# Kernel tuning notes

Measured on AMD Instinct MI355X. Metric: run time of the kernel, lower is better.

## Reference

```python
import jax, jax.numpy as jnp
import numpy as np

MID = 64        # conf.mid_channels
N_INV = 6       # n_layers=8 -> range(1, n_layers-1) -> 6 involution blocks
K = 7           # involution kernel size
GROUP_CH = 16   # RedNet default group_channels
GROUPS = MID // GROUP_CH   # 4
RED = MID // 4             # reduction_ratio = 4 -> 16


def conv2d(x, w, b=None, pad=0):
    out = jax.lax.conv_general_dilated(
        x, w, window_strides=(1, 1), padding=[(pad, pad), (pad, pad)],
        dimension_numbers=('NCHW', 'OIHW', 'NCHW'))
    if b is not None:
        out = out + b[None, :, None, None]
    return out


def extract_patches(x, k):
    # x: (B,C,H,W) -> (B,C,k*k,H,W), same-padded (torch nn.Unfold with pad=k//2)
    p = k // 2
    xp = jnp.pad(x, ((0, 0), (0, 0), (p, p), (p, p)))
    H, W = x.shape[2], x.shape[3]
    slices = [xp[:, :, i:i + H, j:j + W] for i in range(k) for j in range(k)]
    return jnp.stack(slices, axis=2)


def involution(x, red_w, bn_gamma, bn_beta, span_w, span_b):
    # kernel-generation branch: 1x1 conv (no bias) -> BN(eval, mean=0,var=1) -> ReLU -> 1x1 conv
    t = conv2d(x, red_w)                                     # (B,RED,H,W)
    t = bn_gamma[None, :, None, None] * t + bn_beta[None, :, None, None]
    t = jax.nn.relu(t)
    w = conv2d(t, span_w, span_b)                            # (B,K*K*GROUPS,H,W)
    B, _, H, W = w.shape
    w = w.reshape(B, GROUPS, K * K, H, W)
    patches = extract_patches(x, K).reshape(B, GROUPS, GROUP_CH, K * K, H, W)
    out = jnp.einsum('bgkhw,bgckhw->bgchw', w, patches)      # per-pixel dynamic conv
    return out.reshape(B, MID, H, W)


def setup_inputs() -> dict:
    key = jax.random.key(0)
    ks = jax.random.split(key, 12)
    s = 0.05
    inp = {
        'input_tensor': jax.random.normal(ks[0], (1, 3, 128, 128), jnp.float32),
        'conv_in_w': jax.random.normal(ks[1], (MID, 3, 3, 3), jnp.float32) * s,
        'conv_in_b': jax.random.normal(ks[2], (MID,), jnp.float32) * s,
        'red_w': jax.random.normal(ks[3], (N_INV, RED, MID, 1, 1), jnp.float32) * s,
        'bn_gamma': jnp.ones((N_INV, RED), jnp.float32),
        'bn_beta': jnp.zeros((N_INV, RED), jnp.float32),
        'span_w': jax.random.normal(ks[4], (N_INV, K * K * GROUPS, RED, 1, 1), jnp.float32) * s,
        'span_b': jax.random.normal(ks[5], (N_INV, K * K * GROUPS), jnp.float32) * s,
        'conv_out_w': jax.random.normal(ks[6], (12, MID, 3, 3), jnp.float32) * s,
        'conv_out_b': jax.random.normal(ks[7], (12,), jnp.float32) * s,
    }
    return inp


def reference(input_tensor, conv_in_w, conv_in_b, red_w, bn_gamma, bn_beta,
              span_w, span_b, conv_out_w, conv_out_b):
    x = conv2d(input_tensor, conv_in_w, conv_in_b, pad=2)     # (B,MID,H+2,W+2)
    for l in range(N_INV):
        x = jax.nn.relu(involution(x, red_w[l], bn_gamma[l], bn_beta[l],
                                   span_w[l], span_b[l]))
    pixel = conv2d(x, conv_out_w, conv_out_b, pad=0)          # (B,12,H,W)
    # PixelShuffle(2): (B,12,H,W) -> (B,3,2H,2W)
    B, _, H, W = pixel.shape
    out = pixel.reshape(B, 3, 2, 2, H, W).transpose(0, 1, 4, 2, 5, 3)
    return out.reshape(B, 3, 2 * H, 2 * W)
```

## Files before the change

### kernel.cpp

```cpp
#include <hip/hip_runtime.h>


#define HH 130
#define SP 136
#define PPL (SP*SP)
#define GP (PPL*16)
#define XBUF2 (4*GP)
#define TP1 (16900*16)
#define OFF_TA (2*XBUF2)
#define OFF_TB (OFF_TA + 4*TP1)

__global__ __launch_bounds__(256) void conv_in_kernel(
        const float* __restrict__ inf, const float* __restrict__ W,
        const float* __restrict__ b, float* __restrict__ x0,
        float* __restrict__ x1, float* __restrict__ tpA,
        const float* __restrict__ redw0) {
    const int tid = threadIdx.x;
    if (blockIdx.x >= 67) {
        int idx = ((blockIdx.x - 67)*4 + blockIdx.y)*256 + tid;
        if (idx < 3192) {
            int bsel = idx & 1, e = idx >> 1;
            int r, c;
            if (e < 816) { r = e/136; c = e%136; if (r >= 3) r += 130; }
            else { int j = e-816; r = 3 + j/6; int m = j%6; c = (m<3)? m : m+130; }
            float* base = (bsel ? x1 : x0) + ((size_t)r*SP + c)*16;
            float4 z = make_float4(0.f,0.f,0.f,0.f);
            #pragma unroll
            for (int g2 = 0; g2 < 4; ++g2)
                #pragma unroll
                for (int q = 0; q < 4; ++q)
                    *(float4*)(base + (size_t)g2*GP + q*4) = z;
        }
        return;
    }
    __shared__ float wl[448];
    const int g = blockIdx.y;
    for (int i = tid; i < 448; i += 256)
        wl[i] = (i < 432) ? W[g*432 + i] : b[g*16 + (i-432)];
    __syncthreads();
    int px = blockIdx.x*256 + tid;
    int pxc = px < 16900 ? px : 16899;
    int h = pxc/130, w = pxc%130;
    float xv[27];
    #pragma unroll
    for (int i = 0; i < 3; ++i)
      #pragma unroll
      for (int ky = 0; ky < 3; ++ky) {
        int y = h - 2 + ky;
        #pragma unroll
        for (int kx = 0; kx < 3; ++kx) {
            int xx = w - 2 + kx;
            float v = 0.f;
            if ((unsigned)y < 128u && (unsigned)xx < 128u)
                v = inf[i*16384 + y*128 + xx];
            xv[i*9 + ky*3 + kx] = v;
        }
      }
    float acc[16];
    #pragma unroll
    for (int c = 0; c < 16; ++c) {
        float a = wl[432 + c];
        #pragma unroll
        for (int t = 0; t < 27; ++t) a += wl[c*27 + t] * xv[t];
        acc[c] = a;
    }
    if (px < 16900) {
        float* dst = x0 + (size_t)g*GP + ((size_t)(h+3)*SP + (w+3))*16;
        #pragma unroll
        for (int q = 0; q < 4; ++q)
            *(float4*)(dst + q*4) =
                make_float4(acc[q*4], acc[q*4+1], acc[q*4+2], acc[q*4+3]);
        float* td = tpA + (size_t)g*TP1 + (size_t)px*16;
        #pragma unroll
        for (int rq = 0; rq < 4; ++rq) {
            float p0=0.f, p1=0.f, p2=0.f, p3=0.f;
            #pragma unroll
            for (int j = 0; j < 16; ++j) {
                float a = acc[j];
                p0 += redw0[(rq*4+0)*64 + g*16 + j]*a;
                p1 += redw0[(rq*4+1)*64 + g*16 + j]*a;
                p2 += redw0[(rq*4+2)*64 + g*16 + j]*a;
                p3 += redw0[(rq*4+3)*64 + g*16 + j]*a;
            }
            *(float4*)(td + rq*4) = make_float4(p0, p1, p2, p3);
        }
    }
}

#define TL(p, r)  uu[(p)*20 + (r)]
#define WLK(k, p) uu[(k)*68 + (p)]
__global__ __launch_bounds__(256, 5) void e_kernel(
        const float* __restrict__ x,
        const float* __restrict__ tread,
        float* __restrict__ twrite,
        const float* __restrict__ gamma, const float* __restrict__ beta,
        const float* __restrict__ spanw,
        const float* __restrict__ spanb,
        const float* __restrict__ redwn,
        float* __restrict__ xout,
        const int doNext)
{
    __shared__ float xl[4][14][17][4];
    __shared__ float uu[49*68];
    const int wid = blockIdx.x;
    const int slot = wid >> 3;
    const int T = (wid & 7)*37 + (slot >> 2);
    if (T >= 289) return;
    const int g = slot & 3;
    const int ty = (T/17)*8, tx = (T%17)*8;
    const int tid = threadIdx.x;
    const int px = tid & 63;
    const int wv = __builtin_amdgcn_readfirstlane(tid >> 6);
    const int sr = px >> 3, sc = px & 7;

    for (int i = tid; i < 784; i += 256) {
        int q = i & 3, p = i >> 2;
        int r = p / 14, c = p % 14;
        int gr = ty + r, gc = tx + c;
        gr = gr < SP ? gr : SP-1;
        gc = gc < SP ? gc : SP-1;
        float4 v = *(const float4*)(x + (size_t)g*GP
                                    + ((size_t)gr*SP + gc)*16 + q*4);
        *(float4*)&xl[q][r][c][0] = v;
    }

    const int hh = min(ty + sr, HH-1), ww = min(tx + sc, HH-1);
    {
        const size_t toff = ((size_t)hh*HH + ww)*16 + wv*4;
        float4 s = make_float4(0.f,0.f,0.f,0.f);
        #pragma unroll
        for (int gg = 0; gg < 4; ++gg) {
            float4 a = *(const float4*)(tread + (size_t)gg*TP1 + toff);
            s.x += a.x; s.y += a.y; s.z += a.z; s.w += a.w;
        }
        *(float4*)&TL(px, wv*4) = s;
    }
    __syncthreads();

    float t16[16];
    #pragma unroll
    for (int q = 0; q < 4; ++q) {
        float4 v = *(const float4*)&TL(px, q*4);
        t16[q*4+0] = fmaxf(gamma[q*4+0]*v.x + beta[q*4+0], 0.f);
        t16[q*4+1] = fmaxf(gamma[q*4+1]*v.y + beta[q*4+1], 0.f);
        t16[q*4+2] = fmaxf(gamma[q*4+2]*v.z + beta[q*4+2], 0.f);
        t16[q*4+3] = fmaxf(gamma[q*4+3]*v.w + beta[q*4+3], 0.f);
    }
    __syncthreads();

    {
        const float* sw = spanw + g*784;
        const float* sb = spanb + g*49;
        const int k0 = wv ? (wv*12 + 1) : 0;
        #pragma unroll
        for (int j = 0; j < 12; ++j) {
            int k = k0 + j;
            float a = sb[k];
            #pragma unroll
            for (int r = 0; r < 16; ++r) a += sw[k*16 + r] * t16[r];
            WLK(k, px) = a;
        }
        if (wv == 0) {
            float a = sb[12];
            #pragma unroll
            for (int r = 0; r < 16; ++r) a += sw[12*16 + r] * t16[r];
            WLK(12, px) = a;
        }
    }
    __syncthreads();

    const int cq = wv;
    float4 acc = make_float4(0.f, 0.f, 0.f, 0.f);
    #pragma unroll
    for (int i = 0; i < 7; ++i)
        #pragma unroll
        for (int j = 0; j < 7; ++j) {
            float4 xv = *(const float4*)&xl[cq][sr + i][sc + j][0];
            float wk = WLK(i*7 + j, px);
            acc.x += wk*xv.x; acc.y += wk*xv.y;
            acc.z += wk*xv.z; acc.w += wk*xv.w;
        }

    const int h = ty + sr, ww2 = tx + sc;
    const bool valid = (h < HH) && (ww2 < HH);
    float4 o = make_float4(fmaxf(acc.x,0.f), fmaxf(acc.y,0.f),
                           fmaxf(acc.z,0.f), fmaxf(acc.w,0.f));
    if (valid)
        *(float4*)(xout + (size_t)g*GP
                   + ((size_t)(h+3)*SP + (ww2+3))*16 + cq*4) = o;

    if (doNext) {
        float* ol = (float*)xl;
        __syncthreads();
        ol[px*17 + cq*4 + 0] = o.x;
        ol[px*17 + cq*4 + 1] = o.y;
        ol[px*17 + cq*4 + 2] = o.z;
        ol[px*17 + cq*4 + 3] = o.w;
        __syncthreads();
        const int rq = wv;
        float p0=0.f, p1=0.f, p2=0.f, p3=0.f;
        #pragma unroll
        for (int j = 0; j < 16; ++j) {
            float xv = ol[px*17 + j];
            const int c = g*16 + j;
            p0 += redwn[(rq*4+0)*64 + c]*xv;
            p1 += redwn[(rq*4+1)*64 + c]*xv;
            p2 += redwn[(rq*4+2)*64 + c]*xv;
            p3 += redwn[(rq*4+3)*64 + c]*xv;
        }
        if (valid)
            *(float4*)(twrite + (size_t)g*TP1
                       + ((size_t)h*HH + ww2)*16 + rq*4) =
                make_float4(p0, p1, p2, p3);
    }
}

__global__ __launch_bounds__(256) void conv_out_ps_kernel(
        const float* __restrict__ x, const float* __restrict__ W,
        const float* __restrict__ b, float* __restrict__ out)
{
    __shared__ float xh[64*120];
    __shared__ float wl[6912];
    const int tid = threadIdx.x;
    const int ty = blockIdx.y*8, tx = blockIdx.x*8;

    for (int idx = tid; idx < 6912; idx += 256) wl[idx] = W[idx];
    for (int idx = tid; idx < 1600; idx += 256) {
        int g = idx/400, rem = idx%400;
        int p100 = rem>>2, q = rem&3;
        int r = p100/10, cl = p100%10;
        float4 v = *(const float4*)(x + (size_t)g*GP
                     + ((size_t)(ty + r + 3)*SP + tx + cl + 3)*16 + q*4);
        int c0 = g*16 + q*4;
        xh[(c0+0)*120 + r*12 + cl] = v.x;
        xh[(c0+1)*120 + r*12 + cl] = v.y;
        xh[(c0+2)*120 + r*12 + cl] = v.z;
        xh[(c0+3)*120 + r*12 + cl] = v.w;
    }
    __syncthreads();

    const int wave = __builtin_amdgcn_readfirstlane(tid >> 6);
    const int lane = tid & 63;
    const int s = lane >> 2, cq = lane & 3;
    const int sr = s >> 1, pc0 = (s & 1)*4;
    float acc[3][4] = {};

    for (int c = cq*16; c < cq*16 + 16; ++c) {
        #pragma unroll
        for (int ky = 0; ky < 3; ++ky) {
            const float* xb = &xh[c*120 + (sr + ky)*12 + pc0];
            float4 xa = *(const float4*)xb;
            float2 xm = *(const float2*)(xb + 4);
            float xr[6] = {xa.x, xa.y, xa.z, xa.w, xm.x, xm.y};
            #pragma unroll
            for (int oj = 0; oj < 3; ++oj) {
                const float* wp = &wl[((wave*3 + oj)*64 + c)*9 + ky*3];
                #pragma unroll
                for (int kx = 0; kx < 3; ++kx) {
                    float wv = wp[kx];
                    #pragma unroll
                    for (int q = 0; q < 4; ++q)
                        acc[oj][q] += wv * xr[kx + q];
                }
            }
        }
    }

    #pragma unroll
    for (int oj = 0; oj < 3; ++oj)
        #pragma unroll
        for (int q = 0; q < 4; ++q) {
            float v = acc[oj][q];
            v += __shfl_xor(v, 1, 64);
            v += __shfl_xor(v, 2, 64);
            acc[oj][q] = v;
        }

    if (cq == 0) {
        #pragma unroll
        for (int oj = 0; oj < 3; ++oj) {
            int o = wave*3 + oj;
            float bo = b[o];
            int c3 = o >> 2, r = (o >> 1) & 1, s2 = o & 1;
            int h = ty + sr;
            #pragma unroll
            for (int q = 0; q < 4; ++q) {
                int w = tx + pc0 + q;
                out[c3*65536 + (2*h + r)*256 + 2*w + s2] = acc[oj][q] + bo;
            }
        }
    }
}

extern "C" void kernel_launch(void* const* d_in, const int* in_sizes, int n_in,
                              void* d_out, int out_size, void* d_ws, size_t ws_size,
                              hipStream_t stream) {
    const float* inf   = (const float*)d_in[0];
    const float* cinw  = (const float*)d_in[1];
    const float* cinb  = (const float*)d_in[2];
    const float* redw  = (const float*)d_in[3];
    const float* gam   = (const float*)d_in[4];
    const float* bet   = (const float*)d_in[5];
    const float* spw   = (const float*)d_in[6];
    const float* spb   = (const float*)d_in[7];
    const float* cow   = (const float*)d_in[8];
    const float* cob   = (const float*)d_in[9];

    float* ws = (float*)d_ws;
    float* x0 = ws;
    float* x1 = ws + XBUF2;
    float* tA = ws + OFF_TA;
    float* tB = ws + OFF_TB;

    conv_in_kernel<<<dim3(80, 4), 256, 0, stream>>>(
        inf, cinw, cinb, x0, x1, tA, redw);

    float* cur = x0; float* nxt = x1;
    for (int l = 0; l < 6; ++l) {
        const int doNext = (l < 5);
        float* tread  = (l & 1) ? tB : tA;
        float* twrite = (l & 1) ? tA : tB;
        e_kernel<<<1184, 256, 0, stream>>>(
            cur, tread, twrite,
            gam + l*16, bet + l*16,
            spw + l*3136, spb + l*196,
            redw + (doNext ? (l+1)*1024 : 0),
            nxt, doNext);
        float* t = cur; cur = nxt; nxt = t;
    }

    conv_out_ps_kernel<<<dim3(16, 16), 256, 0, stream>>>(
        cur, cow, cob, (float*)d_out);
}
```

Baseline: 190.9 us.

## Widen involution tiles to 8x16 with two output pixels per thread

Each involution block now covers an 8x16 pixel tile, so the 7x7 halo is loaded once for twice as many outputs, and the grid is roughly halved. Each thread computes two adjacent output columns, reusing a sliding window of 8 loaded float4 values from shared memory across both. Per-pixel kernel weights are stored interleaved in pairs so they can be fetched as float4. The cost is more registers, a lower occupancy hint (3 instead of 5 blocks), and fewer blocks to spread across the CUs.

Measured after the change: 342.8 us. 79.6% more time.

```diff
diff --git a/kernel.cpp b/kernel.cpp
--- a/kernel.cpp
+++ b/kernel.cpp
@@ -87,9 +87,9 @@
     }
 }
 
-#define TL(p, r)  uu[(p)*20 + (r)]
-#define WLK(k, p) uu[(k)*68 + (p)]
-__global__ __launch_bounds__(256, 5) void e_kernel(
+#define EHR 14
+#define EHC 24
+__global__ __launch_bounds__(256, 3) void e_kernel(
         const float* __restrict__ x,
         const float* __restrict__ tread,
         float* __restrict__ twrite,
@@ -100,118 +100,152 @@
         float* __restrict__ xout,
         const int doNext)
 {
-    __shared__ float xl[4][14][17][4];
-    __shared__ float uu[49*68];
+    __shared__ float xl[4*EHR*EHC*4];
+    __shared__ float uu2[25*64*4];
     const int wid = blockIdx.x;
-    const int slot = wid >> 3;
-    const int T = (wid & 7)*37 + (slot >> 2);
-    if (T >= 289) return;
-    const int g = slot & 3;
-    const int ty = (T/17)*8, tx = (T%17)*8;
+    const int sid = (wid & 7)*77 + (wid >> 3);
+    if (sid >= 612) return;
+    const int T = sid >> 2, g = sid & 3;
+    const int ty = (T/9)*8, tx = (T%9)*16;
     const int tid = threadIdx.x;
-    const int px = tid & 63;
-    const int wv = __builtin_amdgcn_readfirstlane(tid >> 6);
-    const int sr = px >> 3, sc = px & 7;
-
-    for (int i = tid; i < 784; i += 256) {
+    const int cq = __builtin_amdgcn_readfirstlane(tid >> 6);
+    const int pos = tid & 63;
+    const int posr = pos >> 3, posc = pos & 7;
+
+    for (int i = tid; i < EHR*22*4; i += 256) {
         int q = i & 3, p = i >> 2;
-        int r = p / 14, c = p % 14;
+        int r = p / 22, c = p % 22;
         int gr = ty + r, gc = tx + c;
         gr = gr < SP ? gr : SP-1;
         gc = gc < SP ? gc : SP-1;
         float4 v = *(const float4*)(x + (size_t)g*GP
                                     + ((size_t)gr*SP + gc)*16 + q*4);
-        *(float4*)&xl[q][r][c][0] = v;
-    }
-
-    const int hh = min(ty + sr, HH-1), ww = min(tx + sc, HH-1);
-    {
-        const size_t toff = ((size_t)hh*HH + ww)*16 + wv*4;
+        *(float4*)&xl[((q*EHR + r)*EHC + c)*4] = v;
+    }
+
+    float* tl = uu2;
+    for (int it = 0; it < 2; ++it) {
+        int task = tid + it*256;
+        int pxt = task >> 2, qd = task & 3;
+        int hh = min(ty + (pxt >> 4), HH-1), ww = min(tx + (pxt & 15), HH-1);
+        const size_t toff = ((size_t)hh*HH + ww)*16 + qd*4;
         float4 s = make_float4(0.f,0.f,0.f,0.f);
         #pragma unroll
         for (int gg = 0; gg < 4; ++gg) {
             float4 a = *(const float4*)(tread + (size_t)gg*TP1 + toff);
             s.x += a.x; s.y += a.y; s.z += a.z; s.w += a.w;
         }
-        *(float4*)&TL(px, wv*4) = s;
+        *(float4*)&tl[pxt*20 + qd*4] = s;
     }
     __syncthreads();
 
-    float t16[16];
-    #pragma unroll
-    for (int q = 0; q < 4; ++q) {
-        float4 v = *(const float4*)&TL(px, q*4);
-        t16[q*4+0] = fmaxf(gamma[q*4+0]*v.x + beta[q*4+0], 0.f);
-        t16[q*4+1] = fmaxf(gamma[q*4+1]*v.y + beta[q*4+1], 0.f);
-        t16[q*4+2] = fmaxf(gamma[q*4+2]*v.z + beta[q*4+2], 0.f);
-        t16[q*4+3] = fmaxf(gamma[q*4+3]*v.w + beta[q*4+3], 0.f);
-    }
-    __syncthreads();
-
     {
+        const int pxw = tid & 127;
+        const int sub = __builtin_amdgcn_readfirstlane(tid >> 7);
+        float t16[16];
+        #pragma unroll
+        for (int q = 0; q < 4; ++q) {
+            float4 v = *(const float4*)&tl[pxw*20 + q*4];
+            t16[q*4+0] = fmaxf(gamma[q*4+0]*v.x + beta[q*4+0], 0.f);
+            t16[q*4+1] = fmaxf(gamma[q*4+1]*v.y + beta[q*4+1], 0.f);
+            t16[q*4+2] = fmaxf(gamma[q*4+2]*v.z + beta[q*4+2], 0.f);
+            t16[q*4+3] = fmaxf(gamma[q*4+3]*v.w + beta[q*4+3], 0.f);
+        }
+        __syncthreads();
         const float* sw = spanw + g*784;
         const float* sb = spanb + g*49;
-        const int k0 = wv ? (wv*12 + 1) : 0;
-        #pragma unroll
-        for (int j = 0; j < 12; ++j) {
-            int k = k0 + j;
-            float a = sb[k];
-            #pragma unroll
-            for (int r = 0; r < 16; ++r) a += sw[k*16 + r] * t16[r];
-            WLK(k, px) = a;
-        }
-        if (wv == 0) {
-            float a = sb[12];
-            #pragma unroll
-            for (int r = 0; r < 16; ++r) a += sw[12*16 + r] * t16[r];
-            WLK(12, px) = a;
+        float* wl2 = uu2;
+        const int wslot = (pxw >> 1)*4 + (pxw & 1);
+        for (int it = 0; it < 13; ++it) {
+            int kp = sub + it*2;
+            if (kp < 25) {
+                int k0 = 2*kp, k1 = 2*kp + 1;
+                float a0 = sb[k0];
+                #pragma unroll
+                for (int r = 0; r < 16; ++r) a0 += sw[k0*16 + r] * t16[r];
+                float a1 = 0.f;
+                if (k1 < 49) {
+                    a1 = sb[k1];
+                    #pragma unroll
+                    for (int r = 0; r < 16; ++r) a1 += sw[k1*16 + r] * t16[r];
+                }
+                wl2[kp*256 + wslot]     = a0;
+                wl2[kp*256 + wslot + 2] = a1;
+            }
         }
     }
     __syncthreads();
 
-    const int cq = wv;
-    float4 acc = make_float4(0.f, 0.f, 0.f, 0.f);
+    const float* wl2 = uu2;
+    float4 acc0 = make_float4(0.f,0.f,0.f,0.f);
+    float4 acc1 = make_float4(0.f,0.f,0.f,0.f);
+    const int c0 = posc*2;
     #pragma unroll
-    for (int i = 0; i < 7; ++i)
-        #pragma unroll
-        for (int j = 0; j < 7; ++j) {
-            float4 xv = *(const float4*)&xl[cq][sr + i][sc + j][0];
-            float wk = WLK(i*7 + j, px);
-            acc.x += wk*xv.x; acc.y += wk*xv.y;
-            acc.z += wk*xv.z; acc.w += wk*xv.w;
-        }
-
-    const int h = ty + sr, ww2 = tx + sc;
-    const bool valid = (h < HH) && (ww2 < HH);
-    float4 o = make_float4(fmaxf(acc.x,0.f), fmaxf(acc.y,0.f),
-                           fmaxf(acc.z,0.f), fmaxf(acc.w,0.f));
-    if (valid)
-        *(float4*)(xout + (size_t)g*GP
-                   + ((size_t)(h+3)*SP + (ww2+3))*16 + cq*4) = o;
+    for (int i = 0; i < 7; ++i) {
+        const int row = posr + i;
+        float4 xv[8];
+        #pragma unroll
+        for (int jj = 0; jj < 8; ++jj)
+            xv[jj] = *(const float4*)&xl[((cq*EHR + row)*EHC + c0 + jj)*4];
+        const int kb = (7*i) >> 1;
+        float4 wv[4];
+        #pragma unroll
+        for (int m = 0; m < 4; ++m)
+            wv[m] = *(const float4*)&wl2[(kb + m)*256 + pos*4];
+        #pragma unroll
+        for (int jj = 0; jj < 7; ++jj) {
+            const int k = 7*i + jj;
+            const int m = (k >> 1) - kb, sl = k & 1;
+            float w0 = sl ? ((m==0)?wv[0].z:(m==1)?wv[1].z:(m==2)?wv[2].z:wv[3].z)
+                          : ((m==0)?wv[0].x:(m==1)?wv[1].x:(m==2)?wv[2].x:wv[3].x);
+            float w1 = sl ? ((m==0)?wv[0].w:(m==1)?wv[1].w:(m==2)?wv[2].w:wv[3].w)
+                          : ((m==0)?wv[0].y:(m==1)?wv[1].y:(m==2)?wv[2].y:wv[3].y);
+            acc0.x += w0*xv[jj].x;   acc0.y += w0*xv[jj].y;
+            acc0.z += w0*xv[jj].z;   acc0.w += w0*xv[jj].w;
+            acc1.x += w1*xv[jj+1].x; acc1.y += w1*xv[jj+1].y;
+            acc1.z += w1*xv[jj+1].z; acc1.w += w1*xv[jj+1].w;
+        }
+    }
+
+    const int h = ty + posr;
+    const int w0c = tx + c0, w1c = w0c + 1;
+    const bool v0 = (h < HH) && (w0c < HH);
+    const bool v1 = (h < HH) && (w1c < HH);
+    float4 o0 = make_float4(fmaxf(acc0.x,0.f), fmaxf(acc0.y,0.f),
+                            fmaxf(acc0.z,0.f), fmaxf(acc0.w,0.f));
+    float4 o1 = make_float4(fmaxf(acc1.x,0.f), fmaxf(acc1.y,0.f),
+                            fmaxf(acc1.z,0.f), fmaxf(acc1.w,0.f));
+    if (v0) *(float4*)(xout + (size_t)g*GP
+                       + ((size_t)(h+3)*SP + (w0c+3))*16 + cq*4) = o0;
+    if (v1) *(float4*)(xout + (size_t)g*GP
+                       + ((size_t)(h+3)*SP + (w1c+3))*16 + cq*4) = o1;
 
     if (doNext) {
-        float* ol = (float*)xl;
+        float* ol = xl;
         __syncthreads();
-        ol[px*17 + cq*4 + 0] = o.x;
-        ol[px*17 + cq*4 + 1] = o.y;
-        ol[px*17 + cq*4 + 2] = o.z;
-        ol[px*17 + cq*4 + 3] = o.w;
+        const int px0 = posr*16 + c0;
+        *(float4*)&ol[px0*20 + cq*4]       = o0;
+        *(float4*)&ol[(px0+1)*20 + cq*4]   = o1;
         __syncthreads();
-        const int rq = wv;
-        float p0=0.f, p1=0.f, p2=0.f, p3=0.f;
-        #pragma unroll
-        for (int j = 0; j < 16; ++j) {
-            float xv = ol[px*17 + j];
-            const int c = g*16 + j;
-            p0 += redwn[(rq*4+0)*64 + c]*xv;
-            p1 += redwn[(rq*4+1)*64 + c]*xv;
-            p2 += redwn[(rq*4+2)*64 + c]*xv;
-            p3 += redwn[(rq*4+3)*64 + c]*xv;
-        }
-        if (valid)
-            *(float4*)(twrite + (size_t)g*TP1
-                       + ((size_t)h*HH + ww2)*16 + rq*4) =
-                make_float4(p0, p1, p2, p3);
+        const int rq = cq;
+        for (int it = 0; it < 2; ++it) {
+            int pxr = (tid & 63) | (it << 6);
+            float p0=0.f, p1=0.f, p2=0.f, p3=0.f;
+            #pragma unroll
+            for (int jc = 0; jc < 16; ++jc) {
+                float xv = ol[pxr*20 + jc];
+                const int c = g*16 + jc;
+                p0 += redwn[(rq*4+0)*64 + c]*xv;
+                p1 += redwn[(rq*4+1)*64 + c]*xv;
+                p2 += redwn[(rq*4+2)*64 + c]*xv;
+                p3 += redwn[(rq*4+3)*64 + c]*xv;
+            }
+            int h2 = ty + (pxr >> 4), w2 = tx + (pxr & 15);
+            if (h2 < HH && w2 < HH)
+                *(float4*)(twrite + (size_t)g*TP1
+                           + ((size_t)h2*HH + w2)*16 + rq*4) =
+                    make_float4(p0, p1, p2, p3);
+        }
     }
 }
 
@@ -320,7 +354,7 @@
         const int doNext = (l < 5);
         float* tread  = (l & 1) ? tB : tA;
         float* twrite = (l & 1) ? tA : tB;
-        e_kernel<<<1184, 256, 0, stream>>>(
+        e_kernel<<<616, 256, 0, stream>>>(
             cur, tread, twrite,
             gam + l*16, bet + l*16,
             spw + l*3136, spb + l*196,
```
